# Performance work log

Measured on AMD Instinct MI355X. Metric: run time of the kernel, lower is better.

Reference implementation:

```python
import jax, jax.numpy as jnp
import numpy as np

B, T, C = 4, 2048, 1024
N_HEAD = 16
HEAD_DIM = C // N_HEAD


def setup_inputs() -> dict:
    key = jax.random.key(0)
    k1, k2, k3, k4, k5 = jax.random.split(key, 5)
    s = 0.02
    return {
        "x": jax.random.normal(k1, (B, T, C), dtype=jnp.float32),
        "w_attn": jax.random.normal(k2, (C, 3 * C), dtype=jnp.float32) * s,
        "b_attn": jnp.zeros((3 * C,), dtype=jnp.float32),
        "w_proj": jax.random.normal(k3, (C, C), dtype=jnp.float32) * s,
        "b_proj": jnp.zeros((C,), dtype=jnp.float32),
    }


def reference(x, w_attn, b_attn, w_proj, b_proj):
    Bb, Tt, Cc = x.shape
    qkv = x @ w_attn + b_attn                      # [B,T,3C]
    q, k, v = jnp.split(qkv, 3, axis=-1)
    # [B,T,C] -> [B,H,T,D]
    def heads(t):
        return t.reshape(Bb, Tt, N_HEAD, HEAD_DIM).transpose(0, 2, 1, 3)
    q, k, v = heads(q), heads(k), heads(v)
    scale = 1.0 / (HEAD_DIM ** 0.5)
    att = jnp.einsum('bhqd,bhkd->bhqk', q, k) * scale
    causal = jnp.tril(jnp.ones((Tt, Tt), dtype=bool))
    att = jnp.where(causal, att, -jnp.inf)
    att = jax.nn.softmax(att, axis=-1)             # dropout p=0.0 -> identity
    y = jnp.einsum('bhqk,bhkd->bhqd', att, v)
    y = y.transpose(0, 2, 1, 3).reshape(Bb, Tt, Cc)
    return y @ w_proj + b_proj
```

## Files before the change

### kernel.cpp

```cpp
#include <hip/hip_runtime.h>
#include <hip/hip_bf16.h>

typedef unsigned short u16;
typedef unsigned int u32;
typedef __bf16 bf16_t;
typedef bf16_t bf16x8 __attribute__((ext_vector_type(8)));
typedef float f32x4 __attribute__((ext_vector_type(4)));
typedef u16 u16x4 __attribute__((ext_vector_type(4)));
typedef u32 u32x2 __attribute__((ext_vector_type(2)));
typedef u32 u32x4 __attribute__((ext_vector_type(4)));
typedef int intx2 __attribute__((ext_vector_type(2)));

#define MFMA16(a, b, c) __builtin_amdgcn_mfma_f32_16x16x32_bf16((a), (b), (c), 0, 0, 0)

#define QSCL 0.18033688011112042f

__device__ __forceinline__ u16 f2b(float f) {
  bf16_t h = (bf16_t)f;
  return __builtin_bit_cast(u16, h);
}

__device__ __forceinline__ void gload_lds16(const void* src, void* dst) {
  __builtin_amdgcn_global_load_lds(
      (const __attribute__((address_space(1))) void*)src,
      (__attribute__((address_space(3))) void*)dst, 16, 0, 0);
}

__device__ __forceinline__ bf16x8 frag_read(const u16* tile, int row, int kchunk) {
  int off = row * 128 + ((kchunk ^ (row & 7)) << 4);
  return *reinterpret_cast<const bf16x8*>(reinterpret_cast<const char*>(tile) + off);
}

__device__ __forceinline__ void stage128(const u16* g, int rowStrideElts, u16* tile, int tid) {
  int lane = tid & 63, w = tid >> 6;
#pragma unroll
  for (int i = 0; i < 4; ++i) {
    int r = w * 32 + i * 8 + (lane >> 3);
    int cs = (lane & 7) ^ (r & 7);
    gload_lds16(g + (size_t)r * rowStrideElts + cs * 8, tile + r * 64 + (lane & 7) * 8);
  }
}

__global__ __launch_bounds__(256) void cvt_f32_bf16(const float* __restrict__ in,
                                                    u16* __restrict__ out, int n4) {
  int i = blockIdx.x * 256 + threadIdx.x;
  if (i < n4) {
    float4 f = reinterpret_cast<const float4*>(in)[i];
    ushort4 o;
    o.x = f2b(f.x); o.y = f2b(f.y); o.z = f2b(f.z); o.w = f2b(f.w);
    reinterpret_cast<ushort4*>(out)[i] = o;
  }
}

__global__ __launch_bounds__(256) void transpose_cvt(const float* __restrict__ in,
                                                     u16* __restrict__ out, int K, int N) {
  __shared__ float t[32][33];
  int n0 = blockIdx.x * 32, k0 = blockIdx.y * 32;
  int tx = threadIdx.x & 31, ty = threadIdx.x >> 5;
#pragma unroll
  for (int i = 0; i < 32; i += 8)
    t[ty + i][tx] = in[(size_t)(k0 + ty + i) * N + n0 + tx];
  __syncthreads();
#pragma unroll
  for (int i = 0; i < 32; i += 8)
    out[(size_t)(n0 + ty + i) * K + k0 + tx] = f2b(t[tx][ty + i]);
}

__global__ __launch_bounds__(256) void gemm_qkv(const u16* __restrict__ xb,
                                                const u16* __restrict__ waT,
                                                const float* __restrict__ bias,
                                                u16* __restrict__ q, u16* __restrict__ kk,
                                                u16* __restrict__ vt) {
  __shared__ u16 lA[128 * 64];
  __shared__ u16 lB[128 * 64];
  int tid = threadIdx.x, lane = tid & 63, w = tid >> 6;
  int wr = w >> 1, wc = w & 1;
  int bm = blockIdx.x, bn = blockIdx.y;
  f32x4 acc[4][4] = {};
  const u16* gA = xb + (size_t)bm * 128 * 1024;
  const u16* gB = waT + (size_t)bn * 128 * 1024;
  for (int k0 = 0; k0 < 1024; k0 += 64) {
    stage128(gA + k0, 1024, lA, tid);
    stage128(gB + k0, 1024, lB, tid);
    __syncthreads();
#pragma unroll
    for (int s = 0; s < 2; ++s) {
      bf16x8 af[4], bfr[4];
#pragma unroll
      for (int mi = 0; mi < 4; ++mi)
        af[mi] = frag_read(lA, wr * 64 + mi * 16 + (lane & 15), (lane >> 4) + s * 4);
#pragma unroll
      for (int ni = 0; ni < 4; ++ni)
        bfr[ni] = frag_read(lB, wc * 64 + ni * 16 + (lane & 15), (lane >> 4) + s * 4);
#pragma unroll
      for (int mi = 0; mi < 4; ++mi)
#pragma unroll
        for (int ni = 0; ni < 4; ++ni)
          acc[mi][ni] = MFMA16(af[mi], bfr[ni], acc[mi][ni]);
    }
    __syncthreads();
  }
  int m0 = bm * 128 + wr * 64;
  int n0 = bn * 128 + wc * 64;
#pragma unroll
  for (int ni = 0; ni < 4; ++ni) {
    int col = n0 + ni * 16 + (lane & 15);
    float bv = bias[col];
    int part = col >> 10;
    int cin = col & 1023;
    int h = cin >> 6, d = cin & 63;
    float fct = (part == 0) ? QSCL : 1.0f;
#pragma unroll
    for (int mi = 0; mi < 4; ++mi) {
#pragma unroll
      for (int j = 0; j < 4; ++j) {
        int row = m0 + mi * 16 + (lane >> 4) * 4 + j;
        int b = row >> 11, t = row & 2047;
        u16 hv = f2b((acc[mi][ni][j] + bv) * fct);
        if (part == 0)
          q[(((size_t)(b * 16 + h) * 2048 + t) << 6) + d] = hv;
        else if (part == 1)
          kk[(((size_t)(b * 16 + h) * 2048 + t) << 6) + d] = hv;
        else
          vt[(((size_t)(b * 16 + h) << 6) + d) * 2048 + t] = hv;
      }
    }
  }
}

__global__ __launch_bounds__(256) void gemm_proj(const u16* __restrict__ att,
                                                 const u16* __restrict__ wpT,
                                                 const float* __restrict__ bias,
                                                 float* __restrict__ out) {
  __shared__ u16 lA[128 * 64];
  __shared__ u16 lB[128 * 64];
  int tid = threadIdx.x, lane = tid & 63, w = tid >> 6;
  int wr = w >> 1, wc = w & 1;
  int bm = blockIdx.x, bn = blockIdx.y;
  f32x4 acc[4][4] = {};
  const u16* gA = att + (size_t)bm * 128 * 1024;
  const u16* gB = wpT + (size_t)bn * 128 * 1024;
  for (int k0 = 0; k0 < 1024; k0 += 64) {
    stage128(gA + k0, 1024, lA, tid);
    stage128(gB + k0, 1024, lB, tid);
    __syncthreads();
#pragma unroll
    for (int s = 0; s < 2; ++s) {
      bf16x8 af[4], bfr[4];
#pragma unroll
      for (int mi = 0; mi < 4; ++mi)
        af[mi] = frag_read(lA, wr * 64 + mi * 16 + (lane & 15), (lane >> 4) + s * 4);
#pragma unroll
      for (int ni = 0; ni < 4; ++ni)
        bfr[ni] = frag_read(lB, wc * 64 + ni * 16 + (lane & 15), (lane >> 4) + s * 4);
#pragma unroll
      for (int mi = 0; mi < 4; ++mi)
#pragma unroll
        for (int ni = 0; ni < 4; ++ni)
          acc[mi][ni] = MFMA16(af[mi], bfr[ni], acc[mi][ni]);
    }
    __syncthreads();
  }
  int m0 = bm * 128 + wr * 64;
  int n0 = bn * 128 + wc * 64;
#pragma unroll
  for (int ni = 0; ni < 4; ++ni) {
    int col = n0 + ni * 16 + (lane & 15);
    float bv = bias[col];
#pragma unroll
    for (int mi = 0; mi < 4; ++mi)
#pragma unroll
      for (int j = 0; j < 4; ++j) {
        int row = m0 + mi * 16 + (lane >> 4) * 4 + j;
        out[(size_t)row * 1024 + col] = acc[mi][ni][j] + bv;
      }
  }
}


__device__ __forceinline__ void stage_kv(const u16* kb, const u16* vb, int kt,
                                         u16* lK, u16* lV, int tid) {
  int lane = tid & 63, w = tid >> 6;
#pragma unroll
  for (int i = 0; i < 2; ++i) {
    int r = w * 16 + i * 8 + (lane >> 3);
    int cs = (lane & 7) ^ (r & 7);
    gload_lds16(kb + (size_t)(kt * 64 + r) * 64 + cs * 8, lK + r * 64 + (lane & 7) * 8);
    gload_lds16(vb + (size_t)r * 2048 + kt * 64 + cs * 8, lV + r * 64 + (lane & 7) * 8);
  }
}

__device__ __forceinline__ bf16x8 pdist(u32 a0, u32 a1, u32 b0, u32 b1, bool odd) {
  intx2 r0 = __builtin_amdgcn_permlane32_swap((int)a0, (int)b0, false, false);
  intx2 r1 = __builtin_amdgcn_permlane32_swap((int)a1, (int)b1, false, false);
  u32 x0 = __shfl_xor((u32)r0[1], 16, 64);
  u32 x1 = __shfl_xor((u32)r1[1], 16, 64);
  u32 y0 = __shfl_xor((u32)r0[0], 16, 64);
  u32 y1 = __shfl_xor((u32)r1[0], 16, 64);
  u32x4 f;
  f[0] = odd ? x0 : (u32)r0[0];
  f[1] = odd ? x1 : (u32)r1[0];
  f[2] = odd ? (u32)r0[1] : y0;
  f[3] = odd ? (u32)r1[1] : y1;
  return __builtin_bit_cast(bf16x8, f);
}

__global__ __launch_bounds__(256, 3) void attn_fwd(const u16* __restrict__ q,
                                                   const u16* __restrict__ kk,
                                                   const u16* __restrict__ vt,
                                                   u16* __restrict__ att) {
  __shared__ u16 lK[3][64 * 64];
  __shared__ u16 lV[3][64 * 64];
  int tid = threadIdx.x, lane = tid & 63, w = tid >> 6;
  int ln = lane & 15, g = lane >> 4;
  int gh = g >> 1, gl = g & 1;
  bool godd = (g & 1) != 0;
  int bh = blockIdx.x;
  int qtA = blockIdx.y;
  int qtB = 31 - qtA;
  const u16* qb = q + (size_t)bh * 2048 * 64;
  const u16* kb = kk + (size_t)bh * 2048 * 64;
  const u16* vb = vt + (size_t)bh * 64 * 2048;
  int q0A = qtA * 64 + w * 16;
  int q0B = qtB * 64 + w * 16;

  bf16x8 aqA[2], aqB[2];
  {
    const u16* pa = qb + (size_t)(q0A + ln) * 64 + g * 8;
    const u16* pb = qb + (size_t)(q0B + ln) * 64 + g * 8;
    aqA[0] = *reinterpret_cast<const bf16x8*>(pa);
    aqA[1] = *reinterpret_cast<const bf16x8*>(pa + 32);
    aqB[0] = *reinterpret_cast<const bf16x8*>(pb);
    aqB[1] = *reinterpret_cast<const bf16x8*>(pb + 32);
  }

  float mA = -1e30f, lA = 0.f, mB = -1e30f, lB = 0.f;
  f32x4 oA[4] = {}, oB[4] = {};

  auto softmax_state = [&](f32x4* sf, float& m_r, float& l_r, f32x4* o,
                           bool domask, int k0, int qg,
                           bf16x8& pf0, bf16x8& pf1) {
    if (domask) {
#pragma unroll
      for (int kc = 0; kc < 4; ++kc)
#pragma unroll
        for (int j = 0; j < 4; ++j)
          if (k0 + kc * 16 + g * 4 + j > qg) sf[kc][j] = -1e30f;
    }
    f32x4 m4;
#pragma unroll
    for (int j = 0; j < 4; ++j)
      m4[j] = fmaxf(fmaxf(sf[0][j], sf[1][j]), fmaxf(sf[2][j], sf[3][j]));
    float mxl = fmaxf(fmaxf(m4[0], m4[1]), fmaxf(m4[2], m4[3]));
    if (!__all(mxl - m_r <= 8.f)) {
      float mx = fmaxf(mxl, __shfl_xor(mxl, 16, 64));
      mx = fmaxf(mx, __shfl_xor(mx, 32, 64));
      mx = fmaxf(m_r, mx);
      float sc = __builtin_amdgcn_exp2f(m_r - mx);
      m_r = mx;
      l_r *= sc;
#pragma unroll
      for (int dc = 0; dc < 4; ++dc) o[dc] *= sc;
    }
    u32 d0[4], d1[4];
    float rs = 0.f;
#pragma unroll
    for (int kc = 0; kc < 4; ++kc) {
      u16x4 v4;
#pragma unroll
      for (int j = 0; j < 4; ++j) {
        float p = __builtin_amdgcn_exp2f(sf[kc][j] - m_r);
        rs += p;
        v4[j] = f2b(p);
      }
      u32x2 dd = __builtin_bit_cast(u32x2, v4);
      d0[kc] = dd[0];
      d1[kc] = dd[1];
    }
    l_r += rs;
    pf0 = pdist(d0[0], d1[0], d0[1], d1[1], godd);
    pf1 = pdist(d0[2], d1[2], d0[3], d1[3], godd);
  };

  stage_kv(kb, vb, 0, &lK[0][0], &lV[0][0], tid);
  stage_kv(kb, vb, 1, &lK[1][0], &lV[1][0], tid);

  for (int kt = 0; kt <= qtB; ++kt) {
    if (kt < qtB) {
      asm volatile("s_waitcnt vmcnt(4)" ::: "memory");
    } else {
      asm volatile("s_waitcnt vmcnt(0)" ::: "memory");
    }
    __builtin_amdgcn_s_barrier();
    if (kt + 2 <= qtB) {
      int nb = kt + 2 - ((kt + 2) >= 3 ? 3 : 0);
      nb = (kt + 2) % 3;
      stage_kv(kb, vb, kt + 2, &lK[nb][0], &lV[nb][0], tid);
    }
    int cur = kt % 3;
    const u16* Kt = &lK[cur][0];
    const u16* Vt = &lV[cur][0];
    bool doA = (kt <= qtA);

    f32x4 sB[4], sA[4];
    __builtin_amdgcn_s_setprio(1);
#pragma unroll
    for (int kc = 0; kc < 4; ++kc) {
      f32x4 zB = {}, zA = {};
#pragma unroll
      for (int s = 0; s < 2; ++s) {
        bf16x8 kf = frag_read(Kt, kc * 16 + ln, g + 4 * s);
        zB = MFMA16(kf, aqB[s], zB);
        if (doA) zA = MFMA16(kf, aqA[s], zA);
      }
      sB[kc] = zB;
      sA[kc] = zA;
    }
    __builtin_amdgcn_s_setprio(0);

    bf16x8 vf0[4], vf1[4];
#pragma unroll
    for (int dc = 0; dc < 4; ++dc) {
      vf0[dc] = frag_read(Vt, dc * 16 + ln, g);
      vf1[dc] = frag_read(Vt, dc * 16 + ln, g + 4);
    }

    bf16x8 pB0, pB1, pA0, pA1;
    softmax_state(sB, mB, lB, oB, kt == qtB, kt * 64, q0B + ln, pB0, pB1);
    __builtin_amdgcn_s_setprio(1);
#pragma unroll
    for (int dc = 0; dc < 4; ++dc) {
      oB[dc] = MFMA16(vf0[dc], pB0, oB[dc]);
      oB[dc] = MFMA16(vf1[dc], pB1, oB[dc]);
    }
    __builtin_amdgcn_s_setprio(0);
    if (doA) {
      softmax_state(sA, mA, lA, oA, kt == qtA, kt * 64, q0A + ln, pA0, pA1);
      __builtin_amdgcn_s_setprio(1);
#pragma unroll
      for (int dc = 0; dc < 4; ++dc) {
        oA[dc] = MFMA16(vf0[dc], pA0, oA[dc]);
        oA[dc] = MFMA16(vf1[dc], pA1, oA[dc]);
      }
      __builtin_amdgcn_s_setprio(0);
    }
  }

  __syncthreads();
  u16* lPw = &lK[0][0] + w * 1024;
  int prow = ln * 128;
  int xorq = (ln & 7) << 4;
  int b = bh >> 4, h = bh & 15;
  auto epi = [&](const f32x4* o, float l_r, int q0w) {
    float lt = l_r + __shfl_xor(l_r, 16, 64);
    lt += __shfl_xor(lt, 32, 64);
    float inv = __builtin_amdgcn_rcpf(lt);
#pragma unroll
    for (int dc = 0; dc < 4; ++dc) {
      u16x4 v4;
#pragma unroll
      for (int j = 0; j < 4; ++j) v4[j] = f2b(o[dc][j] * inv);
      *reinterpret_cast<u16x4*>(reinterpret_cast<char*>(lPw) + prow +
                                ((((dc << 1) + gh) << 4) ^ xorq) + gl * 8) = v4;
    }
    asm volatile("s_waitcnt lgkmcnt(0)" ::: "memory");
    __builtin_amdgcn_sched_barrier(0);
    __builtin_amdgcn_wave_barrier();
    bf16x8 r0 = frag_read(lPw, ln, g);
    bf16x8 r1 = frag_read(lPw, ln, g + 4);
    __builtin_amdgcn_sched_barrier(0);
    int t = q0w + ln;
    u16* dst = att + (size_t)(b * 2048 + t) * 1024 + h * 64;
    *reinterpret_cast<bf16x8*>(dst + g * 8) = r0;
    *reinterpret_cast<bf16x8*>(dst + 32 + g * 8) = r1;
  };
  epi(oB, lB, q0B);
  epi(oA, lA, q0A);
}

extern "C" void kernel_launch(void* const* d_in, const int* in_sizes, int n_in,
                              void* d_out, int out_size, void* d_ws, size_t ws_size,
                              hipStream_t stream) {
  const float* x = (const float*)d_in[0];
  const float* w_attn = (const float*)d_in[1];
  const float* b_attn = (const float*)d_in[2];
  const float* w_proj = (const float*)d_in[3];
  const float* b_proj = (const float*)d_in[4];
  float* out = (float*)d_out;

  u16* ws = (u16*)d_ws;
  u16* xb = ws;
  u16* waT = xb + 8388608;
  u16* wpT = waT + 3145728;
  u16* vtx = wpT + 1048576;
  u16* att = xb;
  u16* qx = (u16*)d_out;
  u16* kx = qx + 8388608;

  cvt_f32_bf16<<<8192, 256, 0, stream>>>(x, xb, 2097152);
  transpose_cvt<<<dim3(96, 32), 256, 0, stream>>>(w_attn, waT, 1024, 3072);
  transpose_cvt<<<dim3(32, 32), 256, 0, stream>>>(w_proj, wpT, 1024, 1024);
  gemm_qkv<<<dim3(64, 24), 256, 0, stream>>>(xb, waT, b_attn, qx, kx, vtx);
  attn_fwd<<<dim3(64, 16), 256, 0, stream>>>(qx, kx, vtx, att);
  gemm_proj<<<dim3(64, 8), 256, 0, stream>>>(att, wpT, b_proj, out);
}
```

Measured before the change: 203.4 us.

## Load V fragments directly from global, drop V LDS staging, raise occupancy

The attention kernel no longer stages V tiles through LDS with async global-to-LDS copies. Each wave now reads its V MFMA fragments straight from global memory into registers at the top of each key tile, and only K stays triple-buffered in LDS. This halves LDS usage so launch bounds can go from 3 to 4 blocks per CU, and it simplifies the vmcnt wait logic. The cost is that V loads now have exposed global/L2 latency with strided 16-byte reads, plus higher register pressure from holding the fragments early.

```diff
diff --git a/kernel.cpp b/kernel.cpp
--- a/kernel.cpp
+++ b/kernel.cpp
@@ -178,15 +178,13 @@
 }
 
 
-__device__ __forceinline__ void stage_kv(const u16* kb, const u16* vb, int kt,
-                                         u16* lK, u16* lV, int tid) {
+__device__ __forceinline__ void stage_k(const u16* kb, int kt, u16* lK, int tid) {
   int lane = tid & 63, w = tid >> 6;
 #pragma unroll
   for (int i = 0; i < 2; ++i) {
     int r = w * 16 + i * 8 + (lane >> 3);
     int cs = (lane & 7) ^ (r & 7);
     gload_lds16(kb + (size_t)(kt * 64 + r) * 64 + cs * 8, lK + r * 64 + (lane & 7) * 8);
-    gload_lds16(vb + (size_t)r * 2048 + kt * 64 + cs * 8, lV + r * 64 + (lane & 7) * 8);
   }
 }
 
@@ -205,12 +203,11 @@
   return __builtin_bit_cast(bf16x8, f);
 }
 
-__global__ __launch_bounds__(256, 3) void attn_fwd(const u16* __restrict__ q,
+__global__ __launch_bounds__(256, 4) void attn_fwd(const u16* __restrict__ q,
                                                    const u16* __restrict__ kk,
                                                    const u16* __restrict__ vt,
                                                    u16* __restrict__ att) {
   __shared__ u16 lK[3][64 * 64];
-  __shared__ u16 lV[3][64 * 64];
   int tid = threadIdx.x, lane = tid & 63, w = tid >> 6;
   int ln = lane & 15, g = lane >> 4;
   int gh = g >> 1, gl = g & 1;
@@ -282,24 +279,26 @@
     pf1 = pdist(d0[2], d1[2], d0[3], d1[3], godd);
   };
 
-  stage_kv(kb, vb, 0, &lK[0][0], &lV[0][0], tid);
-  stage_kv(kb, vb, 1, &lK[1][0], &lV[1][0], tid);
+  stage_k(kb, 0, &lK[0][0], tid);
+  stage_k(kb, 1, &lK[1][0], tid);
 
   for (int kt = 0; kt <= qtB; ++kt) {
-    if (kt < qtB) {
-      asm volatile("s_waitcnt vmcnt(4)" ::: "memory");
-    } else {
-      asm volatile("s_waitcnt vmcnt(0)" ::: "memory");
-    }
+    asm volatile("s_waitcnt vmcnt(2)" ::: "memory");
     __builtin_amdgcn_s_barrier();
-    if (kt + 2 <= qtB) {
-      int nb = kt + 2 - ((kt + 2) >= 3 ? 3 : 0);
-      nb = (kt + 2) % 3;
-      stage_kv(kb, vb, kt + 2, &lK[nb][0], &lV[nb][0], tid);
-    }
-    int cur = kt % 3;
-    const u16* Kt = &lK[cur][0];
-    const u16* Vt = &lV[cur][0];
+
+    bf16x8 vf0[4], vf1[4];
+    const u16* vbase = vb + kt * 64;
+#pragma unroll
+    for (int dc = 0; dc < 4; ++dc) {
+      const u16* vr = vbase + (size_t)(dc * 16 + ln) * 2048;
+      vf0[dc] = *reinterpret_cast<const bf16x8*>(vr + g * 8);
+      vf1[dc] = *reinterpret_cast<const bf16x8*>(vr + (g + 4) * 8);
+    }
+    __builtin_amdgcn_sched_barrier(0);
+    if (kt + 2 <= qtB) stage_k(kb, kt + 2, &lK[(kt + 2) % 3][0], tid);
+    __builtin_amdgcn_sched_barrier(0);
+
+    const u16* Kt = &lK[kt % 3][0];
     bool doA = (kt <= qtA);
 
     f32x4 sB[4], sA[4];
@@ -317,13 +316,6 @@
       sA[kc] = zA;
     }
     __builtin_amdgcn_s_setprio(0);
-
-    bf16x8 vf0[4], vf1[4];
-#pragma unroll
-    for (int dc = 0; dc < 4; ++dc) {
-      vf0[dc] = frag_read(Vt, dc * 16 + ln, g);
-      vf1[dc] = frag_read(Vt, dc * 16 + ln, g + 4);
-    }
 
     bf16x8 pB0, pB1, pA0, pA1;
     softmax_state(sB, mB, lB, oB, kt == qtB, kt * 64, q0B + ln, pB0, pB1);
```

After: 355.5 us. +74.7%, slower.

## Stage V-transpose epilogue through LDS and remap GEMM workgroups across XCDs

Applied to the files above, without the earlier changes.

In the QKV GEMM, blocks that produce V now write their tile into swizzled LDS scratch and read it back transposed, so each lane stores 16-byte contiguous runs into vt instead of scattered 2-byte strided stores. Both GEMMs also remap the linear block id so consecutive ids sent to the same XCD share the same bm/bn neighbourhood, aiming at better L2 reuse. The remap assumes fixed grid sizes (64x24 and 64x8), and the LDS scratch reuses the A/B buffers after the main loop, synchronised only with a wave barrier. The attention kernel change is a cosmetic simplification of the staging index.

```diff
diff --git a/kernel.cpp b/kernel.cpp
--- a/kernel.cpp
+++ b/kernel.cpp
@@ -7,6 +7,7 @@
 typedef bf16_t bf16x8 __attribute__((ext_vector_type(8)));
 typedef float f32x4 __attribute__((ext_vector_type(4)));
 typedef u16 u16x4 __attribute__((ext_vector_type(4)));
+typedef u16 u16x8 __attribute__((ext_vector_type(8)));
 typedef u32 u32x2 __attribute__((ext_vector_type(2)));
 typedef u32 u32x4 __attribute__((ext_vector_type(4)));
 typedef int intx2 __attribute__((ext_vector_type(2)));
@@ -71,11 +72,14 @@
                                                 const float* __restrict__ bias,
                                                 u16* __restrict__ q, u16* __restrict__ kk,
                                                 u16* __restrict__ vt) {
-  __shared__ u16 lA[128 * 64];
-  __shared__ u16 lB[128 * 64];
+  __shared__ u16 ldsU[2][128 * 64];
+  u16* lA = ldsU[0];
+  u16* lB = ldsU[1];
   int tid = threadIdx.x, lane = tid & 63, w = tid >> 6;
   int wr = w >> 1, wc = w & 1;
-  int bm = blockIdx.x, bn = blockIdx.y;
+  int orig = blockIdx.x + gridDim.x * blockIdx.y;
+  int wgid = (orig & 7) * 192 + (orig >> 3);
+  int bm = wgid & 63, bn = wgid >> 6;
   f32x4 acc[4][4] = {};
   const u16* gA = xb + (size_t)bm * 128 * 1024;
   const u16* gB = waT + (size_t)bn * 128 * 1024;
@@ -102,27 +106,62 @@
   }
   int m0 = bm * 128 + wr * 64;
   int n0 = bn * 128 + wc * 64;
-#pragma unroll
-  for (int ni = 0; ni < 4; ++ni) {
-    int col = n0 + ni * 16 + (lane & 15);
-    float bv = bias[col];
-    int part = col >> 10;
-    int cin = col & 1023;
-    int h = cin >> 6, d = cin & 63;
-    float fct = (part == 0) ? QSCL : 1.0f;
-#pragma unroll
-    for (int mi = 0; mi < 4; ++mi) {
-#pragma unroll
-      for (int j = 0; j < 4; ++j) {
-        int row = m0 + mi * 16 + (lane >> 4) * 4 + j;
-        int b = row >> 11, t = row & 2047;
-        u16 hv = f2b((acc[mi][ni][j] + bv) * fct);
-        if (part == 0)
-          q[(((size_t)(b * 16 + h) * 2048 + t) << 6) + d] = hv;
-        else if (part == 1)
-          kk[(((size_t)(b * 16 + h) * 2048 + t) << 6) + d] = hv;
-        else
-          vt[(((size_t)(b * 16 + h) << 6) + d) * 2048 + t] = hv;
+  if (bn >= 16) {
+    int ln = lane & 15, g = lane >> 4;
+    int hB = (n0 - 2048) >> 6;
+    u16* scr = ldsU[0] + w * 4096;
+#pragma unroll
+    for (int ni = 0; ni < 4; ++ni) {
+      int d = ni * 16 + ln;
+      float bv = bias[n0 + ni * 16 + ln];
+#pragma unroll
+      for (int mi = 0; mi < 4; ++mi) {
+        u16x4 v4;
+#pragma unroll
+        for (int j = 0; j < 4; ++j) v4[j] = f2b(acc[mi][ni][j] + bv);
+        int c = (mi * 4 + g) ^ (d & 15);
+        *reinterpret_cast<u16x4*>(reinterpret_cast<char*>(scr) + d * 128 + c * 8) = v4;
+      }
+    }
+    asm volatile("s_waitcnt lgkmcnt(0)" ::: "memory");
+    __builtin_amdgcn_sched_barrier(0);
+    __builtin_amdgcn_wave_barrier();
+    int bb = bm >> 4;
+    int t0 = (bm & 15) * 128 + wr * 64 + (lane & 7) * 8;
+#pragma unroll
+    for (int p = 0; p < 8; ++p) {
+      int dr = p * 8 + (lane >> 3);
+      int c0 = (lane & 7) * 2;
+      u16x4 lo = *reinterpret_cast<const u16x4*>(
+          reinterpret_cast<const char*>(scr) + dr * 128 + ((c0 ^ (dr & 15)) * 8));
+      u16x4 hi = *reinterpret_cast<const u16x4*>(
+          reinterpret_cast<const char*>(scr) + dr * 128 + (((c0 + 1) ^ (dr & 15)) * 8));
+      u16x8 o8;
+      o8[0] = lo[0]; o8[1] = lo[1]; o8[2] = lo[2]; o8[3] = lo[3];
+      o8[4] = hi[0]; o8[5] = hi[1]; o8[6] = hi[2]; o8[7] = hi[3];
+      *reinterpret_cast<u16x8*>(vt + ((size_t)(bb * 16 + hB) * 64 + dr) * 2048 + t0) = o8;
+    }
+  } else {
+#pragma unroll
+    for (int ni = 0; ni < 4; ++ni) {
+      int col = n0 + ni * 16 + (lane & 15);
+      float bv = bias[col];
+      int part = col >> 10;
+      int cin = col & 1023;
+      int h = cin >> 6, d = cin & 63;
+      float fct = (part == 0) ? QSCL : 1.0f;
+#pragma unroll
+      for (int mi = 0; mi < 4; ++mi) {
+#pragma unroll
+        for (int j = 0; j < 4; ++j) {
+          int row = m0 + mi * 16 + (lane >> 4) * 4 + j;
+          int b = row >> 11, t = row & 2047;
+          u16 hv = f2b((acc[mi][ni][j] + bv) * fct);
+          if (part == 0)
+            q[(((size_t)(b * 16 + h) * 2048 + t) << 6) + d] = hv;
+          else
+            kk[(((size_t)(b * 16 + h) * 2048 + t) << 6) + d] = hv;
+        }
       }
     }
   }
@@ -136,7 +175,9 @@
   __shared__ u16 lB[128 * 64];
   int tid = threadIdx.x, lane = tid & 63, w = tid >> 6;
   int wr = w >> 1, wc = w & 1;
-  int bm = blockIdx.x, bn = blockIdx.y;
+  int orig = blockIdx.x + gridDim.x * blockIdx.y;
+  int wgid = (orig & 7) * 64 + (orig >> 3);
+  int bm = wgid & 63, bn = wgid >> 6;
   f32x4 acc[4][4] = {};
   const u16* gA = att + (size_t)bm * 128 * 1024;
   const u16* gB = wpT + (size_t)bn * 128 * 1024;
@@ -292,11 +333,8 @@
       asm volatile("s_waitcnt vmcnt(0)" ::: "memory");
     }
     __builtin_amdgcn_s_barrier();
-    if (kt + 2 <= qtB) {
-      int nb = kt + 2 - ((kt + 2) >= 3 ? 3 : 0);
-      nb = (kt + 2) % 3;
-      stage_kv(kb, vb, kt + 2, &lK[nb][0], &lV[nb][0], tid);
-    }
+    if (kt + 2 <= qtB)
+      stage_kv(kb, vb, kt + 2, &lK[(kt + 2) % 3][0], &lV[(kt + 2) % 3][0], tid);
     int cur = kt % 3;
     const u16* Kt = &lK[cur][0];
     const u16* Vt = &lV[cur][0];
```

After: 200.5 us. No clear change (-1.4%).
